# Kernel optimization log

Hardware: AMD Instinct MI355X
Metric: run time of the kernel (lower is better)

Reference implementation:

```python
import jax, jax.numpy as jnp
import numpy as np

TEMP = 0.07
W00 = 0.1
EPS = 1e-8


def setup_inputs() -> dict:
    key = jax.random.key(0)
    k1, k2, k3, k4 = jax.random.split(key, 4)
    B, N, D = 32, 256, 256
    M = B * N
    return {
        "audio_feats": jax.random.normal(k1, (B, N, D), dtype=jnp.float32),
        "visual_feats": jax.random.normal(k2, (B, N, D), dtype=jnp.float32),
        "audio_labels": jax.random.randint(k3, (M,), 0, 2, dtype=jnp.int64)
            if jax.config.jax_enable_x64 else jax.random.randint(k3, (M,), 0, 2, dtype=jnp.int32),
        "visual_labels": jax.random.randint(k4, (M,), 0, 2, dtype=jnp.int64)
            if jax.config.jax_enable_x64 else jax.random.randint(k4, (M,), 0, 2, dtype=jnp.int32),
    }


def reference(audio_feats, visual_feats, audio_labels, visual_labels):
    B, N, D = audio_feats.shape
    M = B * N
    a = audio_feats.reshape(M, D)
    v = visual_feats.reshape(M, D)
    # L2 normalize (torch F.normalize uses eps=1e-12 clamp on norm)
    a = a / jnp.maximum(jnp.linalg.norm(a, axis=-1, keepdims=True), 1e-12)
    v = v / jnp.maximum(jnp.linalg.norm(v, axis=-1, keepdims=True), 1e-12)
    sim = (a @ v.T) / TEMP  # (M, M)
    exp_sim = jnp.exp(sim)
    la = audio_labels[:, None]  # (M, 1)
    lv = visual_labels[None, :]  # (1, M)
    pos_mask = (la == lv) & ((la == 1) | (la == 0))
    weight = jnp.where(la == 1, 1.0, W00) * pos_mask.astype(sim.dtype)  # (M, M)
    wexp = exp_sim * weight

    # audio -> visual (row direction)
    denom_a2v = exp_sim.sum(axis=1)
    num_a2v = wexp.sum(axis=1)
    frac_a2v = (num_a2v + EPS) / (denom_a2v + EPS)
    valid_a2v = (num_a2v > 0).astype(sim.dtype)
    loss_a2v = -(valid_a2v * jnp.log(frac_a2v)).sum() / jnp.maximum(valid_a2v.sum(), 1.0)

    # visual -> audio (column direction)
    denom_v2a = exp_sim.sum(axis=0)
    num_v2a = wexp.sum(axis=0)
    frac_v2a = (num_v2a + EPS) / (denom_v2a + EPS)
    valid_v2a = (num_v2a > 0).astype(sim.dtype)
    loss_v2a = -(valid_v2a * jnp.log(frac_v2a)).sum() / jnp.maximum(valid_v2a.sum(), 1.0)

    return 0.5 * (loss_a2v + loss_v2a)
```

## Files before the change

kernel.cpp:

```cpp
#include <hip/hip_runtime.h>

#define M_ROWS 8192
#define D_DIM  256
#define BM     128
#define BN     64
#define NBI    (M_ROWS / BM)
#define NBJ    (M_ROWS / BN)
#define NJOBS  (NBI * NBJ)

#define ALPHA  4.53982478f


typedef __attribute__((ext_vector_type(4))) float floatx4;
typedef __attribute__((ext_vector_type(2))) float floatx2;
typedef __attribute__((ext_vector_type(8))) int   intx8;

#define GLOAD_LDS16(gp, lp) \
    __builtin_amdgcn_global_load_lds( \
        (__attribute__((address_space(1))) void*)(gp), \
        (__attribute__((address_space(3))) void*)(lp), 16, 0, 0)

__device__ inline float fast_exp2(float x) {
#if __has_builtin(__builtin_amdgcn_exp2f)
    return __builtin_amdgcn_exp2f(x);
#else
    return exp2f(x);
#endif
}

__device__ inline floatx4 mfma_fp8(intx8 a, intx8 b, floatx4 c) {
    return __builtin_amdgcn_mfma_scale_f32_16x16x128_f8f6f4(
        a, b, c, 0, 0, 0, 0x7f7f7f7f, 0, 0x7f7f7f7f);
}

__global__ __launch_bounds__(256) void normalize_kernel(
    const float* __restrict__ af, const float* __restrict__ vf,
    unsigned char* __restrict__ aB, unsigned char* __restrict__ vB,
    float* __restrict__ glob)
{
    __shared__ float ssb[16][4];

    if (blockIdx.x == 0) {
        if (threadIdx.x < 4) glob[threadIdx.x] = 0.f;
        if (threadIdx.x == 4) ((int*)glob)[4] = 0;
    }

    const int b = blockIdx.x;
    const bool isA = b < 512;
    const int T = isA ? b : b - 512;
    const float* src = (isA ? af : vf) + (size_t)T * 16 * D_DIM;
    unsigned char* dst = (isA ? aB : vB) + (size_t)T * 4096;

    const int t    = threadIdx.x;
    const int wave = t >> 6, lane = t & 63;
    const int row  = t & 15;
    const int kq   = (t >> 4) & 3;
    const int h    = (t >> 6) & 1;
    const int s    = t >> 7;
    const int kbase = s * 128 + kq * 32 + h * 16;

    const float* p = src + row * D_DIM + kbase;
    float4 x0 = ((const float4*)p)[0], x1 = ((const float4*)p)[1];
    float4 x2 = ((const float4*)p)[2], x3 = ((const float4*)p)[3];

    float ss = x0.x*x0.x + x0.y*x0.y + x0.z*x0.z + x0.w*x0.w
             + x1.x*x1.x + x1.y*x1.y + x1.z*x1.z + x1.w*x1.w
             + x2.x*x2.x + x2.y*x2.y + x2.z*x2.z + x2.w*x2.w
             + x3.x*x3.x + x3.y*x3.y + x3.z*x3.z + x3.w*x3.w;
    ss += __shfl_xor(ss, 16, 64);
    ss += __shfl_xor(ss, 32, 64);
    if (lane < 16) ssb[lane][wave] = ss;
    __syncthreads();
    float tot = ssb[row][0] + ssb[row][1] + ssb[row][2] + ssb[row][3];
    float scale = ALPHA / fmaxf(sqrtf(tot), 1e-12f);

    int4 o;
    int pk;
    pk  = __builtin_amdgcn_cvt_pk_fp8_f32(x0.x*scale, x0.y*scale, 0, false);
    pk  = __builtin_amdgcn_cvt_pk_fp8_f32(x0.z*scale, x0.w*scale, pk, true);
    o.x = pk;
    pk  = __builtin_amdgcn_cvt_pk_fp8_f32(x1.x*scale, x1.y*scale, 0, false);
    pk  = __builtin_amdgcn_cvt_pk_fp8_f32(x1.z*scale, x1.w*scale, pk, true);
    o.y = pk;
    pk  = __builtin_amdgcn_cvt_pk_fp8_f32(x2.x*scale, x2.y*scale, 0, false);
    pk  = __builtin_amdgcn_cvt_pk_fp8_f32(x2.z*scale, x2.w*scale, pk, true);
    o.z = pk;
    pk  = __builtin_amdgcn_cvt_pk_fp8_f32(x3.x*scale, x3.y*scale, 0, false);
    pk  = __builtin_amdgcn_cvt_pk_fp8_f32(x3.z*scale, x3.w*scale, pk, true);
    o.w = pk;
    *(int4*)(dst + (size_t)t * 16) = o;
}

__global__ __launch_bounds__(256, 4) void gemm_loss_kernel(
    const unsigned char* __restrict__ aB, const unsigned char* __restrict__ vB,
    const int* __restrict__ la, const int* __restrict__ lv,
    float* __restrict__ rowPart, float* __restrict__ colPart)
{
    __shared__ __align__(16) unsigned char ldsB[16384];
    __shared__ floatx2 colbuf[4][BN];

    const int tid  = threadIdx.x;
    const int wave = tid >> 6, lane = tid & 63;
    const int quad = lane >> 4, l16 = lane & 15;

    const int bx = blockIdx.x & 63;
    const int by = blockIdx.x >> 6;
    const int i0 = bx * BM, j0 = by * BN;

    {
        const unsigned char* vsrc = vB + (size_t)by * 16384 + (size_t)tid * 16;
        unsigned char* ldst = ldsB + tid * 16;
        #pragma unroll
        for (int c = 0; c < 4; ++c)
            GLOAD_LDS16(vsrc + c * 4096, ldst + c * 4096);
    }

    const unsigned char* Abase = aB + (size_t)(bx * 8 + wave * 2) * 4096
                                    + (size_t)lane * 16;
    intx8 afr[2][2];
    #pragma unroll
    for (int it = 0; it < 2; ++it) {
        #pragma unroll
        for (int s = 0; s < 2; ++s) {
            int4 h0 = *(const int4*)(Abase + it * 4096 + s * 2048);
            int4 h1 = *(const int4*)(Abase + it * 4096 + s * 2048 + 1024);
            afr[it][s] = intx8{h0.x, h0.y, h0.z, h0.w, h1.x, h1.y, h1.z, h1.w};
        }
    }

    __syncthreads();

    floatx4 acc[2][4] = {};
    const unsigned char* Bl = ldsB + lane * 16;
    #pragma unroll
    for (int s = 0; s < 2; ++s) {
        #pragma unroll
        for (int jt = 0; jt < 4; ++jt) {
            int4 h0 = *(const int4*)(Bl + jt * 4096 + s * 2048);
            int4 h1 = *(const int4*)(Bl + jt * 4096 + s * 2048 + 1024);
            intx8 bf = intx8{h0.x, h0.y, h0.z, h0.w, h1.x, h1.y, h1.z, h1.w};
            acc[0][jt] = mfma_fp8(afr[0][s], bf, acc[0][jt]);
            acc[1][jt] = mfma_fp8(afr[1][s], bf, acc[1][jt]);
        }
    }

    const int baseRow = i0 + wave * 32;
    floatx2 ma2[2][4];
    #pragma unroll
    for (int it = 0; it < 2; ++it)
        #pragma unroll
        for (int r = 0; r < 4; ++r)
            ma2[it][r] = floatx2{1.f, (float)la[baseRow + it * 16 + quad * 4 + r]};
    floatx2 mr2[4];
    #pragma unroll
    for (int jt = 0; jt < 4; ++jt)
        mr2[jt] = floatx2{1.f, (float)lv[j0 + jt * 16 + l16]};

    floatx2 rowacc[2][4] = {};
    floatx2 colacc[4] = {};
    #pragma unroll
    for (int it = 0; it < 2; ++it) {
        #pragma unroll
        for (int jt = 0; jt < 4; ++jt) {
            #pragma unroll
            for (int r = 0; r < 4; ++r) {
                float e = fast_exp2(acc[it][jt][r]);
                floatx2 e2 = {e, e};
                rowacc[it][r] = e2 * mr2[jt] + rowacc[it][r];
                colacc[jt]   = e2 * ma2[it][r] + colacc[jt];
            }
        }
    }

    __syncthreads();

    floatx2* rp = (floatx2*)ldsB;
    #pragma unroll
    for (int it = 0; it < 2; ++it)
        #pragma unroll
        for (int r = 0; r < 4; ++r)
            rp[(wave * 32 + it * 16 + quad * 4 + r) * 16 + l16] = rowacc[it][r];

    #pragma unroll
    for (int jt = 0; jt < 4; ++jt) {
        floatx2 v = colacc[jt];
        v.x += __shfl_xor(v.x, 16, 64); v.y += __shfl_xor(v.y, 16, 64);
        v.x += __shfl_xor(v.x, 32, 64); v.y += __shfl_xor(v.y, 32, 64);
        if (quad == 0) colbuf[wave][jt * 16 + l16] = v;
    }
    __syncthreads();

    {
        const int row = tid >> 1, h = tid & 1;
        const float4* b4 = (const float4*)(rp + (size_t)row * 16 + h * 8);
        float4 q0 = b4[0], q1 = b4[1], q2 = b4[2], q3 = b4[3];
        floatx2 s = floatx2{q0.x, q0.y} + floatx2{q0.z, q0.w}
                  + floatx2{q1.x, q1.y} + floatx2{q1.z, q1.w}
                  + floatx2{q2.x, q2.y} + floatx2{q2.z, q2.w}
                  + floatx2{q3.x, q3.y} + floatx2{q3.z, q3.w};
        s.x += __shfl_xor(s.x, 1, 64);
        s.y += __shfl_xor(s.y, 1, 64);
        if (h == 0)
            *(floatx2*)&rowPart[((size_t)by * M_ROWS + i0 + row) * 2] = s;

        if (tid < BN) {
            floatx2 c = colbuf[0][tid] + colbuf[1][tid]
                      + colbuf[2][tid] + colbuf[3][tid];
            *(floatx2*)&colPart[((size_t)bx * M_ROWS + j0 + tid) * 2] = c;
        }
    }
}

__global__ __launch_bounds__(256) void reduce_kernel(
    const float* __restrict__ rowPart, const float* __restrict__ colPart,
    const int* __restrict__ la, const int* __restrict__ lv,
    float* __restrict__ glob, float* __restrict__ out)
{
    const int bid = blockIdx.x;
    const bool aside = bid < 32;
    const int idx = (aside ? bid : bid - 32) * 256 + threadIdx.x;
    const float* part = aside ? rowPart : colPart;
    const int* lab = aside ? la : lv;
    const int nslab = aside ? NBJ : NBI;

    float tot = 0.f, c1 = 0.f;
    #pragma unroll 4
    for (int b = 0; b < nslab; ++b) {
        float2 p = *(const float2*)(part + ((size_t)b * M_ROWS + idx) * 2);
        tot += p.x; c1 += p.y;
    }
    float num = lab[idx] ? c1 : 0.1f * (tot - c1);
    float lg = 0.f, cnt = 0.f;
    if (num > 0.f) { lg = logf((num + 1e-8f) / (tot + 1e-8f)); cnt = 1.f; }

    #pragma unroll
    for (int m = 1; m < 64; m <<= 1) {
        lg  += __shfl_xor(lg,  m, 64);
        cnt += __shfl_xor(cnt, m, 64);
    }
    __shared__ float red[4][2];
    const int w = threadIdx.x >> 6, ln = threadIdx.x & 63;
    if (ln == 0) { red[w][0] = lg; red[w][1] = cnt; }
    __syncthreads();
    if (threadIdx.x == 0) {
        float slg  = red[0][0] + red[1][0] + red[2][0] + red[3][0];
        float scnt = red[0][1] + red[1][1] + red[2][1] + red[3][1];
        float* base = glob + (aside ? 0 : 2);
        atomicAdd(&base[0], slg);
        atomicAdd(&base[1], scnt);
        __threadfence();
        int old = atomicAdd((int*)glob + 4, 1);
        if (old == 63) {
            __threadfence();
            float sA = atomicAdd(&glob[0], 0.f);
            float cA = atomicAdd(&glob[1], 0.f);
            float sV = atomicAdd(&glob[2], 0.f);
            float cV = atomicAdd(&glob[3], 0.f);
            float lossA = -sA / fmaxf(cA, 1.f);
            float lossV = -sV / fmaxf(cV, 1.f);
            out[0] = 0.5f * (lossA + lossV);
        }
    }
}

extern "C" void kernel_launch(void* const* d_in, const int* in_sizes, int n_in,
                              void* d_out, int out_size, void* d_ws, size_t ws_size,
                              hipStream_t stream)
{
    const float* af = (const float*)d_in[0];
    const float* vf = (const float*)d_in[1];
    const int*   la = (const int*)d_in[2];
    const int*   lv = (const int*)d_in[3];
    float* out = (float*)d_out;

    char* ws = (char*)d_ws;
    unsigned char* aB = (unsigned char*)ws;
    unsigned char* vB = (unsigned char*)(ws + 2ull * 1024 * 1024);
    float* rowPart   = (float*)(ws +  4ull * 1024 * 1024);
    float* colPart   = (float*)(ws + 12ull * 1024 * 1024);
    float* glob      = (float*)(ws + 16ull * 1024 * 1024);

    normalize_kernel<<<1024, 256, 0, stream>>>(af, vf, aB, vB, glob);
    gemm_loss_kernel<<<NJOBS, 256, 0, stream>>>(aB, vB, la, lv, rowPart, colPart);
    reduce_kernel<<<64, 256, 0, stream>>>(rowPart, colPart, la, lv, glob, out);
}
```

Before: 116.4 us.

## Process four column tiles per block with double-buffered LDS prefetch

Each block now covers 256 columns instead of 64, looping over four 64-column tiles while prefetching the next V tile into a second LDS buffer. The A fragments stay in registers and are reused across the four tiles. Row partials shrink fourfold, which cuts rowPart traffic and the reduce kernel's slab count. The cost is more LDS per block, occupancy lowered to 3 blocks per CU, and a barrier after every tile.

```diff
diff --git a/kernel.cpp b/kernel.cpp
--- a/kernel.cpp
+++ b/kernel.cpp
@@ -5,8 +5,8 @@
 #define BM     128
 #define BN     64
 #define NBI    (M_ROWS / BM)
-#define NBJ    (M_ROWS / BN)
-#define NJOBS  (NBI * NBJ)
+#define NJQ    (M_ROWS / 256)
+#define NJOBS  (NBI * NJQ)
 
 #define ALPHA  4.53982478f
 
@@ -91,28 +91,77 @@
     *(int4*)(dst + (size_t)t * 16) = o;
 }
 
-__global__ __launch_bounds__(256, 4) void gemm_loss_kernel(
+#define GEMM_STEP(T, LDSRD, LDSWR, DOSTAGE)                                    \
+    {                                                                          \
+        if (DOSTAGE) {                                                         \
+            const unsigned char* vsrc_ = vB + (size_t)(jq * 4 + (T) + 1) * 16384 \
+                                            + (size_t)tid * 16;                \
+            unsigned char* ld_ = (LDSWR) + tid * 16;                           \
+            GLOAD_LDS16(vsrc_,         ld_);                                   \
+            GLOAD_LDS16(vsrc_ +  4096, ld_ +  4096);                           \
+            GLOAD_LDS16(vsrc_ +  8192, ld_ +  8192);                           \
+            GLOAD_LDS16(vsrc_ + 12288, ld_ + 12288);                           \
+        }                                                                      \
+        const unsigned char* Bl_ = (LDSRD) + lane * 16;                        \
+        _Pragma("unroll")                                                      \
+        for (int jt = 0; jt < 4; ++jt) {                                       \
+            int4 h0a = *(const int4*)(Bl_ + jt * 4096);                        \
+            int4 h1a = *(const int4*)(Bl_ + jt * 4096 + 1024);                 \
+            int4 h0b = *(const int4*)(Bl_ + jt * 4096 + 2048);                 \
+            int4 h1b = *(const int4*)(Bl_ + jt * 4096 + 3072);                 \
+            intx8 bf0 = intx8{h0a.x,h0a.y,h0a.z,h0a.w,h1a.x,h1a.y,h1a.z,h1a.w};\
+            intx8 bf1 = intx8{h0b.x,h0b.y,h0b.z,h0b.w,h1b.x,h1b.y,h1b.z,h1b.w};\
+            floatx4 a0 = {}, a1 = {};                                          \
+            a0 = mfma_fp8(afr[0][0], bf0, a0);                                 \
+            a0 = mfma_fp8(afr[0][1], bf1, a0);                                 \
+            a1 = mfma_fp8(afr[1][0], bf0, a1);                                 \
+            a1 = mfma_fp8(afr[1][1], bf1, a1);                                 \
+            floatx2 mj_ = floatx2{1.f,                                         \
+                (float)lv[j0 + (T) * 64 + jt * 16 + l16]};                     \
+            floatx2 ca_ = {};                                                  \
+            _Pragma("unroll")                                                  \
+            for (int r = 0; r < 4; ++r) {                                      \
+                float e0 = fast_exp2(a0[r]);                                   \
+                floatx2 e02 = {e0, e0};                                        \
+                rowacc[0][r] = e02 * mj_ + rowacc[0][r];                       \
+                ca_ = e02 * ma2[0][r] + ca_;                                   \
+                float e1 = fast_exp2(a1[r]);                                   \
+                floatx2 e12 = {e1, e1};                                        \
+                rowacc[1][r] = e12 * mj_ + rowacc[1][r];                       \
+                ca_ = e12 * ma2[1][r] + ca_;                                   \
+            }                                                                  \
+            ca_.x += __shfl_xor(ca_.x, 16, 64);                                \
+            ca_.y += __shfl_xor(ca_.y, 16, 64);                                \
+            ca_.x += __shfl_xor(ca_.x, 32, 64);                                \
+            ca_.y += __shfl_xor(ca_.y, 32, 64);                                \
+            if (quad == 0) colbuf[(T)][wave][jt * 16 + l16] = ca_;             \
+        }                                                                      \
+    }
+
+__global__ __launch_bounds__(256, 3) void gemm_loss_kernel(
     const unsigned char* __restrict__ aB, const unsigned char* __restrict__ vB,
     const int* __restrict__ la, const int* __restrict__ lv,
     float* __restrict__ rowPart, float* __restrict__ colPart)
 {
-    __shared__ __align__(16) unsigned char ldsB[16384];
-    __shared__ floatx2 colbuf[4][BN];
+    __shared__ __align__(16) unsigned char ldsB0[16384];
+    __shared__ __align__(16) unsigned char ldsB1[16384];
+    __shared__ floatx2 colbuf[4][4][64];
 
     const int tid  = threadIdx.x;
     const int wave = tid >> 6, lane = tid & 63;
     const int quad = lane >> 4, l16 = lane & 15;
 
     const int bx = blockIdx.x & 63;
-    const int by = blockIdx.x >> 6;
-    const int i0 = bx * BM, j0 = by * BN;
+    const int jq = blockIdx.x >> 6;
+    const int i0 = bx * BM, j0 = jq * 256;
 
     {
-        const unsigned char* vsrc = vB + (size_t)by * 16384 + (size_t)tid * 16;
-        unsigned char* ldst = ldsB + tid * 16;
-        #pragma unroll
-        for (int c = 0; c < 4; ++c)
-            GLOAD_LDS16(vsrc + c * 4096, ldst + c * 4096);
+        const unsigned char* vsrc = vB + (size_t)(jq * 4) * 16384 + (size_t)tid * 16;
+        unsigned char* ld = ldsB0 + tid * 16;
+        GLOAD_LDS16(vsrc,         ld);
+        GLOAD_LDS16(vsrc +  4096, ld +  4096);
+        GLOAD_LDS16(vsrc +  8192, ld +  8192);
+        GLOAD_LDS16(vsrc + 12288, ld + 12288);
     }
 
     const unsigned char* Abase = aB + (size_t)(bx * 8 + wave * 2) * 4096
@@ -128,22 +177,6 @@
         }
     }
 
-    __syncthreads();
-
-    floatx4 acc[2][4] = {};
-    const unsigned char* Bl = ldsB + lane * 16;
-    #pragma unroll
-    for (int s = 0; s < 2; ++s) {
-        #pragma unroll
-        for (int jt = 0; jt < 4; ++jt) {
-            int4 h0 = *(const int4*)(Bl + jt * 4096 + s * 2048);
-            int4 h1 = *(const int4*)(Bl + jt * 4096 + s * 2048 + 1024);
-            intx8 bf = intx8{h0.x, h0.y, h0.z, h0.w, h1.x, h1.y, h1.z, h1.w};
-            acc[0][jt] = mfma_fp8(afr[0][s], bf, acc[0][jt]);
-            acc[1][jt] = mfma_fp8(afr[1][s], bf, acc[1][jt]);
-        }
-    }
-
     const int baseRow = i0 + wave * 32;
     floatx2 ma2[2][4];
     #pragma unroll
@@ -151,43 +184,26 @@
         #pragma unroll
         for (int r = 0; r < 4; ++r)
             ma2[it][r] = floatx2{1.f, (float)la[baseRow + it * 16 + quad * 4 + r]};
-    floatx2 mr2[4];
-    #pragma unroll
-    for (int jt = 0; jt < 4; ++jt)
-        mr2[jt] = floatx2{1.f, (float)lv[j0 + jt * 16 + l16]};
 
     floatx2 rowacc[2][4] = {};
-    floatx2 colacc[4] = {};
-    #pragma unroll
-    for (int it = 0; it < 2; ++it) {
-        #pragma unroll
-        for (int jt = 0; jt < 4; ++jt) {
-            #pragma unroll
-            for (int r = 0; r < 4; ++r) {
-                float e = fast_exp2(acc[it][jt][r]);
-                floatx2 e2 = {e, e};
-                rowacc[it][r] = e2 * mr2[jt] + rowacc[it][r];
-                colacc[jt]   = e2 * ma2[it][r] + colacc[jt];
-            }
-        }
-    }
-
-    __syncthreads();
-
-    floatx2* rp = (floatx2*)ldsB;
+
+    __syncthreads();
+
+    GEMM_STEP(0, ldsB0, ldsB1, 1)
+    __syncthreads();
+    GEMM_STEP(1, ldsB1, ldsB0, 1)
+    __syncthreads();
+    GEMM_STEP(2, ldsB0, ldsB1, 1)
+    __syncthreads();
+    GEMM_STEP(3, ldsB1, ldsB0, 0)
+    __syncthreads();
+
+    floatx2* rp = (floatx2*)ldsB0;
     #pragma unroll
     for (int it = 0; it < 2; ++it)
         #pragma unroll
         for (int r = 0; r < 4; ++r)
             rp[(wave * 32 + it * 16 + quad * 4 + r) * 16 + l16] = rowacc[it][r];
-
-    #pragma unroll
-    for (int jt = 0; jt < 4; ++jt) {
-        floatx2 v = colacc[jt];
-        v.x += __shfl_xor(v.x, 16, 64); v.y += __shfl_xor(v.y, 16, 64);
-        v.x += __shfl_xor(v.x, 32, 64); v.y += __shfl_xor(v.y, 32, 64);
-        if (quad == 0) colbuf[wave][jt * 16 + l16] = v;
-    }
     __syncthreads();
 
     {
@@ -201,13 +217,12 @@
         s.x += __shfl_xor(s.x, 1, 64);
         s.y += __shfl_xor(s.y, 1, 64);
         if (h == 0)
-            *(floatx2*)&rowPart[((size_t)by * M_ROWS + i0 + row) * 2] = s;
-
-        if (tid < BN) {
-            floatx2 c = colbuf[0][tid] + colbuf[1][tid]
-                      + colbuf[2][tid] + colbuf[3][tid];
-            *(floatx2*)&colPart[((size_t)bx * M_ROWS + j0 + tid) * 2] = c;
-        }
+            *(floatx2*)&rowPart[((size_t)jq * M_ROWS + i0 + row) * 2] = s;
+
+        const int st = tid >> 6, cl = tid & 63;
+        floatx2 c = colbuf[st][0][cl] + colbuf[st][1][cl]
+                  + colbuf[st][2][cl] + colbuf[st][3][cl];
+        *(floatx2*)&colPart[((size_t)bx * M_ROWS + j0 + tid) * 2] = c;
     }
 }
 
@@ -221,7 +236,7 @@
     const int idx = (aside ? bid : bid - 32) * 256 + threadIdx.x;
     const float* part = aside ? rowPart : colPart;
     const int* lab = aside ? la : lv;
-    const int nslab = aside ? NBJ : NBI;
+    const int nslab = aside ? NJQ : NBI;
 
     float tot = 0.f, c1 = 0.f;
     #pragma unroll 4
@@ -277,8 +292,8 @@
     unsigned char* aB = (unsigned char*)ws;
     unsigned char* vB = (unsigned char*)(ws + 2ull * 1024 * 1024);
     float* rowPart   = (float*)(ws +  4ull * 1024 * 1024);
-    float* colPart   = (float*)(ws + 12ull * 1024 * 1024);
-    float* glob      = (float*)(ws + 16ull * 1024 * 1024);
+    float* colPart   = (float*)(ws +  8ull * 1024 * 1024);
+    float* glob      = (float*)(ws + 12ull * 1024 * 1024);
 
     normalize_kernel<<<1024, 256, 0, stream>>>(af, vf, aB, vB, glob);
     gemm_loss_kernel<<<NJOBS, 256, 0, stream>>>(aB, vB, la, lv, rowPart, colPart);
```

After: 282.1 us. 2.42x slower.

## Double GEMM tile to 256x128 with 512-thread blocks and supertile swizzle

Applied to the files above, without the earlier changes.

Doubles the block tile to 256 rows by 128 columns with 8 waves per block, so each block reuses a larger LDS B tile and writes fewer partial sums. Blocks are remapped into 16x16 supertiles to improve L2 locality. The async global-to-LDS loads are replaced by ordinary register loads and stores, and column reductions are done per column tile to lower register pressure. The risks are a quarter as many blocks, hence less occupancy and parallelism, plus losing the direct-to-LDS load path.

```diff
diff --git a/kernel.cpp b/kernel.cpp
--- a/kernel.cpp
+++ b/kernel.cpp
@@ -2,8 +2,8 @@
 
 #define M_ROWS 8192
 #define D_DIM  256
-#define BM     128
-#define BN     64
+#define BM     256
+#define BN     128
 #define NBI    (M_ROWS / BM)
 #define NBJ    (M_ROWS / BN)
 #define NJOBS  (NBI * NBJ)
@@ -14,11 +14,6 @@
 typedef __attribute__((ext_vector_type(4))) float floatx4;
 typedef __attribute__((ext_vector_type(2))) float floatx2;
 typedef __attribute__((ext_vector_type(8))) int   intx8;
-
-#define GLOAD_LDS16(gp, lp) \
-    __builtin_amdgcn_global_load_lds( \
-        (__attribute__((address_space(1))) void*)(gp), \
-        (__attribute__((address_space(3))) void*)(lp), 16, 0, 0)
 
 __device__ inline float fast_exp2(float x) {
 #if __has_builtin(__builtin_amdgcn_exp2f)
@@ -91,31 +86,33 @@
     *(int4*)(dst + (size_t)t * 16) = o;
 }
 
-__global__ __launch_bounds__(256, 4) void gemm_loss_kernel(
+__global__ __launch_bounds__(512, 4) void gemm_loss_kernel(
     const unsigned char* __restrict__ aB, const unsigned char* __restrict__ vB,
     const int* __restrict__ la, const int* __restrict__ lv,
     float* __restrict__ rowPart, float* __restrict__ colPart)
 {
-    __shared__ __align__(16) unsigned char ldsB[16384];
-    __shared__ floatx2 colbuf[4][BN];
+    __shared__ __align__(16) unsigned char ldsB[32768];
+    __shared__ floatx2 colbuf[8][BN];
 
     const int tid  = threadIdx.x;
     const int wave = tid >> 6, lane = tid & 63;
     const int quad = lane >> 4, l16 = lane & 15;
 
-    const int bx = blockIdx.x & 63;
-    const int by = blockIdx.x >> 6;
+    const int super = blockIdx.x >> 8;
+    const int inner = blockIdx.x & 255;
+    const int bx = (super & 1) * 16 + (inner & 15);
+    const int by = (super >> 1) * 16 + (inner >> 4);
     const int i0 = bx * BM, j0 = by * BN;
 
     {
-        const unsigned char* vsrc = vB + (size_t)by * 16384 + (size_t)tid * 16;
+        const unsigned char* vsrc = vB + (size_t)by * 32768 + (size_t)tid * 16;
         unsigned char* ldst = ldsB + tid * 16;
         #pragma unroll
         for (int c = 0; c < 4; ++c)
-            GLOAD_LDS16(vsrc + c * 4096, ldst + c * 4096);
-    }
-
-    const unsigned char* Abase = aB + (size_t)(bx * 8 + wave * 2) * 4096
+            *(int4*)(ldst + c * 8192) = *(const int4*)(vsrc + c * 8192);
+    }
+
+    const unsigned char* Abase = aB + (size_t)(bx * 16 + wave * 2) * 4096
                                     + (size_t)lane * 16;
     intx8 afr[2][2];
     #pragma unroll
@@ -130,12 +127,12 @@
 
     __syncthreads();
 
-    floatx4 acc[2][4] = {};
+    floatx4 acc[2][8] = {};
     const unsigned char* Bl = ldsB + lane * 16;
     #pragma unroll
     for (int s = 0; s < 2; ++s) {
         #pragma unroll
-        for (int jt = 0; jt < 4; ++jt) {
+        for (int jt = 0; jt < 8; ++jt) {
             int4 h0 = *(const int4*)(Bl + jt * 4096 + s * 2048);
             int4 h1 = *(const int4*)(Bl + jt * 4096 + s * 2048 + 1024);
             intx8 bf = intx8{h0.x, h0.y, h0.z, h0.w, h1.x, h1.y, h1.z, h1.w};
@@ -151,25 +148,25 @@
         #pragma unroll
         for (int r = 0; r < 4; ++r)
             ma2[it][r] = floatx2{1.f, (float)la[baseRow + it * 16 + quad * 4 + r]};
-    floatx2 mr2[4];
-    #pragma unroll
-    for (int jt = 0; jt < 4; ++jt)
-        mr2[jt] = floatx2{1.f, (float)lv[j0 + jt * 16 + l16]};
 
     floatx2 rowacc[2][4] = {};
-    floatx2 colacc[4] = {};
-    #pragma unroll
-    for (int it = 0; it < 2; ++it) {
-        #pragma unroll
-        for (int jt = 0; jt < 4; ++jt) {
+    #pragma unroll
+    for (int jt = 0; jt < 8; ++jt) {
+        floatx2 mj = floatx2{1.f, (float)lv[j0 + jt * 16 + l16]};
+        floatx2 ca = {};
+        #pragma unroll
+        for (int it = 0; it < 2; ++it) {
             #pragma unroll
             for (int r = 0; r < 4; ++r) {
                 float e = fast_exp2(acc[it][jt][r]);
                 floatx2 e2 = {e, e};
-                rowacc[it][r] = e2 * mr2[jt] + rowacc[it][r];
-                colacc[jt]   = e2 * ma2[it][r] + colacc[jt];
+                rowacc[it][r] = e2 * mj + rowacc[it][r];
+                ca = e2 * ma2[it][r] + ca;
             }
         }
+        ca.x += __shfl_xor(ca.x, 16, 64); ca.y += __shfl_xor(ca.y, 16, 64);
+        ca.x += __shfl_xor(ca.x, 32, 64); ca.y += __shfl_xor(ca.y, 32, 64);
+        if (quad == 0) colbuf[wave][jt * 16 + l16] = ca;
     }
 
     __syncthreads();
@@ -180,14 +177,6 @@
         #pragma unroll
         for (int r = 0; r < 4; ++r)
             rp[(wave * 32 + it * 16 + quad * 4 + r) * 16 + l16] = rowacc[it][r];
-
-    #pragma unroll
-    for (int jt = 0; jt < 4; ++jt) {
-        floatx2 v = colacc[jt];
-        v.x += __shfl_xor(v.x, 16, 64); v.y += __shfl_xor(v.y, 16, 64);
-        v.x += __shfl_xor(v.x, 32, 64); v.y += __shfl_xor(v.y, 32, 64);
-        if (quad == 0) colbuf[wave][jt * 16 + l16] = v;
-    }
     __syncthreads();
 
     {
@@ -204,8 +193,9 @@
             *(floatx2*)&rowPart[((size_t)by * M_ROWS + i0 + row) * 2] = s;
 
         if (tid < BN) {
-            floatx2 c = colbuf[0][tid] + colbuf[1][tid]
-                      + colbuf[2][tid] + colbuf[3][tid];
+            floatx2 c = colbuf[0][tid] + colbuf[1][tid] + colbuf[2][tid]
+                      + colbuf[3][tid] + colbuf[4][tid] + colbuf[5][tid]
+                      + colbuf[6][tid] + colbuf[7][tid];
             *(floatx2*)&colPart[((size_t)bx * M_ROWS + j0 + tid) * 2] = c;
         }
     }
@@ -221,7 +211,7 @@
     const int idx = (aside ? bid : bid - 32) * 256 + threadIdx.x;
     const float* part = aside ? rowPart : colPart;
     const int* lab = aside ? la : lv;
-    const int nslab = aside ? NBJ : NBI;
+    const int nslab = aside ? 64 : 32;
 
     float tot = 0.f, c1 = 0.f;
     #pragma unroll 4
@@ -277,10 +267,10 @@
     unsigned char* aB = (unsigned char*)ws;
     unsigned char* vB = (unsigned char*)(ws + 2ull * 1024 * 1024);
     float* rowPart   = (float*)(ws +  4ull * 1024 * 1024);
-    float* colPart   = (float*)(ws + 12ull * 1024 * 1024);
-    float* glob      = (float*)(ws + 16ull * 1024 * 1024);
+    float* colPart   = (float*)(ws +  8ull * 1024 * 1024);
+    float* glob      = (float*)(ws + 12ull * 1024 * 1024);
 
     normalize_kernel<<<1024, 256, 0, stream>>>(af, vf, aB, vB, glob);
-    gemm_loss_kernel<<<NJOBS, 256, 0, stream>>>(aB, vB, la, lv, rowPart, colPart);
+    gemm_loss_kernel<<<NJOBS, 512, 0, stream>>>(aB, vB, la, lv, rowPart, colPart);
     reduce_kernel<<<64, 256, 0, stream>>>(rowPart, colPart, la, lv, glob, out);
 }
```

Measured after the change: 255.7 us. 120% more time.
